# Kernel optimization log

Hardware: AMD Instinct MI355X
Metric: run time of the kernel (lower is better)

Reference implementation:

```python
import jax, jax.numpy as jnp
import numpy as np

IN_F = 4096
OUT_F = 4096
GROUPSIZE = 128
NUM_GROUPS = IN_F // GROUPSIZE  # 32


def setup_inputs() -> dict:
    key = jax.random.key(0)
    k1, k2, k3, k4 = jax.random.split(key, 4)
    x = jax.random.normal(k1, (4, 2048, IN_F), dtype=jnp.float32)
    imin = jnp.iinfo(jnp.int32).min
    imax = jnp.iinfo(jnp.int32).max
    qweight = jax.random.randint(k2, (IN_F // 8, OUT_F), imin, imax, dtype=jnp.int32)
    qzeros = jax.random.randint(k3, (NUM_GROUPS, OUT_F // 8), imin, imax, dtype=jnp.int32)
    scales = jax.random.uniform(k4, (NUM_GROUPS, OUT_F), dtype=jnp.float32,
                                minval=1e-3, maxval=2e-2)
    return {"x": x, "qweight": qweight, "qzeros": qzeros, "scales": scales}


def _unpack_rows(q):
    # q: int32 [in/8, out] -> float nibbles [in, out]; nibble i of a word is bits 4i..4i+3
    u = q.astype(jnp.uint32)
    shifts = (4 * jnp.arange(8, dtype=jnp.uint32))[None, :, None]  # [1,8,1]
    nib = (u[:, None, :] >> shifts) & jnp.uint32(0xF)              # [in/8, 8, out]
    return nib.reshape(q.shape[0] * 8, q.shape[1]).astype(jnp.float32)


def _unpack_cols(q):
    # q: int32 [g, out/8] -> float nibbles [g, out]
    u = q.astype(jnp.uint32)
    shifts = (4 * jnp.arange(8, dtype=jnp.uint32))[None, None, :]  # [1,1,8]
    nib = (u[:, :, None] >> shifts) & jnp.uint32(0xF)              # [g, out/8, 8]
    return nib.reshape(q.shape[0], q.shape[1] * 8).astype(jnp.float32)


def _dequant(qweight, qzeros, scales):
    # GPTQ dequant: w = scale[g] * (q - (z[g] + 1))
    q = _unpack_rows(qweight)                      # [IN_F, OUT_F]
    z = _unpack_cols(qzeros) + 1.0                 # [G, OUT_F]
    qg = q.reshape(NUM_GROUPS, GROUPSIZE, OUT_F)
    w = (qg - z[:, None, :]) * scales[:, None, :]
    return w.reshape(IN_F, OUT_F)


def reference(x, qweight, qzeros, scales):
    w = _dequant(qweight, qzeros, scales)          # [IN_F, OUT_F]
    # x: [B, S, IN_F] @ w -> [B, S, OUT_F]
    return jnp.einsum('bsi,io->bso', x, w)
```

## Files before the change

kernel.cpp:

```cpp
#include <hip/hip_runtime.h>
#include <stdint.h>

#define IN_F   4096
#define OUT_F  4096
#define M_ROWS 8192
#define KT     (IN_F / 64)

typedef __attribute__((ext_vector_type(8))) short  bf16x8;
typedef __attribute__((ext_vector_type(4))) float  f32x4;

__device__ __forceinline__ short f2bf(float f) {
    union { float f; uint32_t u; } v; v.f = f;
    uint32_t r = v.u + 0x7FFFu + ((v.u >> 16) & 1u);
    return (short)(r >> 16);
}

__device__ __forceinline__ void load_lds16(const void* gsrc, void* lds) {
    __builtin_amdgcn_global_load_lds(
        (const __attribute__((address_space(1))) uint32_t*)gsrc,
        (__attribute__((address_space(3))) uint32_t*)lds,
        16, 0, 0);
}

__global__ void dequant_wt_kernel(const int* __restrict__ qweight,
                                  const int* __restrict__ qzeros,
                                  const float* __restrict__ scales,
                                  short* __restrict__ wt)
{
    int t  = blockIdx.x * blockDim.x + threadIdx.x;
    int n  = t >> 9;
    int kw = t & 511;
    int g  = kw >> 4;

    float s = scales[g * OUT_F + n];
    uint32_t zw = (uint32_t)qzeros[g * (OUT_F / 8) + (n >> 3)];
    float z1 = (float)((zw >> (4 * (n & 7))) & 0xFu) + 1.0f;
    uint32_t q = (uint32_t)qweight[kw * OUT_F + n];

    bf16x8 out;
#pragma unroll
    for (int i = 0; i < 8; ++i) {
        float w = s * ((float)((q >> (4 * i)) & 0xFu) - z1);
        out[i] = f2bf(w);
    }
    *reinterpret_cast<bf16x8*>(&wt[(size_t)n * IN_F + kw * 8]) = out;
}

__global__ void xconv_kernel(const float* __restrict__ x, short* __restrict__ xb)
{
    int t = blockIdx.x * blockDim.x + threadIdx.x;
    const float4* src = reinterpret_cast<const float4*>(x) + (size_t)t * 2;
    float4 a = src[0], b = src[1];
    bf16x8 h;
    h[0] = f2bf(a.x); h[1] = f2bf(a.y); h[2] = f2bf(a.z); h[3] = f2bf(a.w);
    h[4] = f2bf(b.x); h[5] = f2bf(b.y); h[6] = f2bf(b.z); h[7] = f2bf(b.w);
    reinterpret_cast<bf16x8*>(xb)[t] = h;
}

__global__ __launch_bounds__(512, 2) void gemm8_kernel(
    const short* __restrict__ Xb,
    const short* __restrict__ WT,
    float* __restrict__ C)
{
    __shared__ short As[2][256 * 64];
    __shared__ short Bs[2][256 * 64];

    const int tid  = threadIdx.x;
    const int lane = tid & 63;
    const int wid  = tid >> 6;
    const int wr   = wid >> 2;
    const int wc   = wid & 3;

    const int row0 = blockIdx.y * 256;
    const int col0 = blockIdx.x * 256;

    const int rL0 = tid >> 3;
    const int csw = ((tid & 7) << 3) ^ ((rL0 & 7) << 3);
    const short* gA[4]; const short* gB[4]; int dOff[4];
#pragma unroll
    for (int L = 0; L < 4; ++L) {
        const int r = L * 64 + rL0;
        gA[L] = Xb + (size_t)(row0 + r) * IN_F + csw;
        gB[L] = WT + (size_t)(col0 + r) * IN_F + csw;
        dOff[L] = L * 8192 + tid * 16;
    }

    const int frow = lane & 15;
    const int k0   = ((lane >> 4) << 4) ^ ((frow & 7) << 4);

    f32x4 acc[8][4] = {};

#pragma unroll
    for (int L = 0; L < 4; ++L) load_lds16(gA[L], (char*)As[0] + dOff[L]);
#pragma unroll
    for (int L = 0; L < 4; ++L) load_lds16(gB[L], (char*)Bs[0] + dOff[L]);
    asm volatile("s_waitcnt vmcnt(0)" ::: "memory");
    __builtin_amdgcn_s_barrier();

    for (int t = 0; t < KT; ++t) {
        const int s = t & 1;
        char* Ab = (char*)As[s];
        char* Bb = (char*)Bs[s];
        char* An = (char*)As[s ^ 1];
        char* Bn = (char*)Bs[s ^ 1];
        const bool pf = (t < KT - 1);

#pragma unroll
        for (int q = 0; q < 4; ++q) {
            const int mq = q >> 1, nq = q & 1;

            bf16x8 af[4][2]; bf16x8 bfr[2][2];
#pragma unroll
            for (int m = 0; m < 4; ++m) {
                const int r = wr * 128 + (mq * 4 + m) * 16 + frow;
                char* base = Ab + r * 128;
                af[m][0] = *reinterpret_cast<const bf16x8*>(base + k0);
                af[m][1] = *reinterpret_cast<const bf16x8*>(base + (k0 ^ 64));
            }
#pragma unroll
            for (int n = 0; n < 2; ++n) {
                const int r = wc * 64 + (nq * 2 + n) * 16 + frow;
                char* base = Bb + r * 128;
                bfr[n][0] = *reinterpret_cast<const bf16x8*>(base + k0);
                bfr[n][1] = *reinterpret_cast<const bf16x8*>(base + (k0 ^ 64));
            }

            if (q == 0 && pf) {
#pragma unroll
                for (int L = 0; L < 4; ++L)
                    load_lds16(gA[L] + (size_t)(t + 1) * 64, An + dOff[L]);
            }
            if (q == 1 && pf) {
#pragma unroll
                for (int L = 0; L < 4; ++L)
                    load_lds16(gB[L] + (size_t)(t + 1) * 64, Bn + dOff[L]);
            }

            __builtin_amdgcn_s_barrier();
            asm volatile("s_waitcnt lgkmcnt(0)" ::: "memory");
            __builtin_amdgcn_sched_barrier(0);

            __builtin_amdgcn_s_setprio(1);
#pragma unroll
            for (int m = 0; m < 4; ++m)
#pragma unroll
                for (int n = 0; n < 2; ++n) {
                    acc[mq * 4 + m][nq * 2 + n] =
                        __builtin_amdgcn_mfma_f32_16x16x32_bf16(
                            af[m][0], bfr[n][0], acc[mq * 4 + m][nq * 2 + n], 0, 0, 0);
                    acc[mq * 4 + m][nq * 2 + n] =
                        __builtin_amdgcn_mfma_f32_16x16x32_bf16(
                            af[m][1], bfr[n][1], acc[mq * 4 + m][nq * 2 + n], 0, 0, 0);
                }
            __builtin_amdgcn_s_setprio(0);

            if (q == 3 && pf)
                asm volatile("s_waitcnt vmcnt(0)" ::: "memory");
            __builtin_amdgcn_s_barrier();
        }
    }

    const int crow = (lane >> 4) * 4;
    const int ccol = lane & 15;
#pragma unroll
    for (int fm = 0; fm < 8; ++fm)
#pragma unroll
        for (int fn = 0; fn < 4; ++fn)
#pragma unroll
            for (int r = 0; r < 4; ++r) {
                const int row = row0 + wr * 128 + fm * 16 + crow + r;
                const int col = col0 + wc * 64 + fn * 16 + ccol;
                C[(size_t)row * OUT_F + col] = acc[fm][fn][r];
            }
}

#define BM 128
#define BN 128
#define BK 64

__global__ __launch_bounds__(256, 2) void gemm_x_wt_kernel(
    const float* __restrict__ X,
    const short* __restrict__ WT,
    float* __restrict__ C)
{
    __shared__ short As2[BM * BK];
    __shared__ short Bs2[BN * BK];

    const int bn = blockIdx.x;
    const int bm = blockIdx.y;
    const int tid  = threadIdx.x;
    const int lane = tid & 63;
    const int wid  = tid >> 6;
    const int wr   = wid >> 1;
    const int wc   = wid & 1;

    const int row0 = bm * BM;
    const int col0 = bn * BN;
    const int frow = lane & 15;
    const int fk   = (lane >> 4) * 8;

    f32x4 acc[4][4] = {};

    for (int kt = 0; kt < IN_F / BK; ++kt) {
        float4 a0[4], a1[4];
#pragma unroll
        for (int j = 0; j < 4; ++j) {
            const int flat = (j * 256 + tid) * 8;
            const int r = flat >> 6;
            const int c = flat & (BK - 1);
            const float* src = X + (size_t)(row0 + r) * IN_F + kt * BK + c;
            a0[j] = *reinterpret_cast<const float4*>(src);
            a1[j] = *reinterpret_cast<const float4*>(src + 4);
        }
        __syncthreads();
#pragma unroll
        for (int j = 0; j < 4; ++j) {
            const int flat = (j * 256 + tid) * 8;
            const int r = flat >> 6;
            const int c = flat & (BK - 1);
            load_lds16(WT + (size_t)(col0 + r) * IN_F + kt * BK + c, &Bs2[flat]);
        }
#pragma unroll
        for (int j = 0; j < 4; ++j) {
            const int flat = (j * 256 + tid) * 8;
            bf16x8 h;
            h[0] = f2bf(a0[j].x); h[1] = f2bf(a0[j].y);
            h[2] = f2bf(a0[j].z); h[3] = f2bf(a0[j].w);
            h[4] = f2bf(a1[j].x); h[5] = f2bf(a1[j].y);
            h[6] = f2bf(a1[j].z); h[7] = f2bf(a1[j].w);
            *reinterpret_cast<bf16x8*>(&As2[flat]) = h;
        }
        __syncthreads();
#pragma unroll
        for (int s = 0; s < 2; ++s) {
            bf16x8 af[4], bfr[4];
#pragma unroll
            for (int m = 0; m < 4; ++m) {
                const int row = wr * 64 + m * 16 + frow;
                af[m] = *reinterpret_cast<const bf16x8*>(&As2[row * BK + s * 32 + fk]);
            }
#pragma unroll
            for (int n = 0; n < 4; ++n) {
                const int col = wc * 64 + n * 16 + frow;
                bfr[n] = *reinterpret_cast<const bf16x8*>(&Bs2[col * BK + s * 32 + fk]);
            }
#pragma unroll
            for (int m = 0; m < 4; ++m)
#pragma unroll
                for (int n = 0; n < 4; ++n)
                    acc[m][n] = __builtin_amdgcn_mfma_f32_16x16x32_bf16(
                        af[m], bfr[n], acc[m][n], 0, 0, 0);
        }
    }

    const int crow = (lane >> 4) * 4;
    const int ccol = lane & 15;
#pragma unroll
    for (int m = 0; m < 4; ++m)
#pragma unroll
        for (int n = 0; n < 4; ++n)
#pragma unroll
            for (int r = 0; r < 4; ++r) {
                const int row = row0 + wr * 64 + m * 16 + crow + r;
                const int col = col0 + wc * 64 + n * 16 + ccol;
                C[(size_t)row * OUT_F + col] = acc[m][n][r];
            }
}

extern "C" void kernel_launch(void* const* d_in, const int* in_sizes, int n_in,
                              void* d_out, int out_size, void* d_ws, size_t ws_size,
                              hipStream_t stream) {
    const float* x       = (const float*)d_in[0];
    const int*   qweight = (const int*)  d_in[1];
    const int*   qzeros  = (const int*)  d_in[2];
    const float* scales  = (const float*)d_in[3];
    float*       out     = (float*)d_out;

    const size_t WT_BYTES = (size_t)OUT_F * IN_F * 2;
    const size_t XB_BYTES = (size_t)M_ROWS * IN_F * 2;

    short* wt = (short*)d_ws;

    dequant_wt_kernel<<<(OUT_F * (IN_F / 8)) / 256, 256, 0, stream>>>(
        qweight, qzeros, scales, wt);

    if (ws_size >= WT_BYTES + XB_BYTES) {
        short* xb = (short*)((char*)d_ws + WT_BYTES);
        xconv_kernel<<<(M_ROWS * IN_F / 8) / 256, 256, 0, stream>>>(x, xb);
        dim3 grid(OUT_F / 256, M_ROWS / 256);
        gemm8_kernel<<<grid, 512, 0, stream>>>(xb, wt, out);
    } else {
        dim3 grid(OUT_F / BN, M_ROWS / BM);
        gemm_x_wt_kernel<<<grid, 256, 0, stream>>>(x, wt, out);
    }
}
```

Baseline: 318.1 us.

## Triple-buffer A tiles to prefetch two K-steps ahead in GEMM

Result: slower. 350.6 us (+10.2%).

```diff
diff --git a/kernel.cpp b/kernel.cpp
--- a/kernel.cpp
+++ b/kernel.cpp
@@ -57,13 +57,18 @@
     reinterpret_cast<bf16x8*>(xb)[t] = h;
 }
 
-__global__ __launch_bounds__(512, 2) void gemm8_kernel(
+#define A_SLOT 32768
+#define B_SLOT 32768
+
+__global__ __launch_bounds__(512, 1) void gemm8_kernel(
     const short* __restrict__ Xb,
     const short* __restrict__ WT,
     float* __restrict__ C)
 {
-    __shared__ short As[2][256 * 64];
-    __shared__ short Bs[2][256 * 64];
+    __shared__ short AsBuf[3 * 256 * 64];
+    __shared__ short BsBuf[2 * 256 * 64];
+    char* const Abase = (char*)AsBuf;
+    char* const Bbase = (char*)BsBuf;
 
     const int tid  = threadIdx.x;
     const int lane = tid & 63;
@@ -91,19 +96,25 @@
     f32x4 acc[8][4] = {};
 
 #pragma unroll
-    for (int L = 0; L < 4; ++L) load_lds16(gA[L], (char*)As[0] + dOff[L]);
-#pragma unroll
-    for (int L = 0; L < 4; ++L) load_lds16(gB[L], (char*)Bs[0] + dOff[L]);
-    asm volatile("s_waitcnt vmcnt(0)" ::: "memory");
+    for (int L = 0; L < 4; ++L) load_lds16(gA[L],      Abase + 0 * A_SLOT + dOff[L]);
+#pragma unroll
+    for (int L = 0; L < 4; ++L) load_lds16(gB[L],      Bbase + 0 * B_SLOT + dOff[L]);
+#pragma unroll
+    for (int L = 0; L < 4; ++L) load_lds16(gA[L] + 64, Abase + 1 * A_SLOT + dOff[L]);
+    asm volatile("s_waitcnt vmcnt(4)" ::: "memory");
     __builtin_amdgcn_s_barrier();
 
+    int sA = 0;
+    int sB = 0;
+
     for (int t = 0; t < KT; ++t) {
-        const int s = t & 1;
-        char* Ab = (char*)As[s];
-        char* Bb = (char*)Bs[s];
-        char* An = (char*)As[s ^ 1];
-        char* Bn = (char*)Bs[s ^ 1];
-        const bool pf = (t < KT - 1);
+        char* Ab = Abase + sA * A_SLOT;
+        char* Bb = Bbase + sB * B_SLOT;
+        const int sA2 = (sA >= 1) ? sA - 1 : 2;
+        char* An = Abase + sA2 * A_SLOT;
+        char* Bn = Bbase + (sB ^ 1) * B_SLOT;
+        const bool pfB = (t + 1 < KT);
+        const bool pfA = (t + 2 < KT);
 
 #pragma unroll
         for (int q = 0; q < 4; ++q) {
@@ -125,15 +136,15 @@
                 bfr[n][1] = *reinterpret_cast<const bf16x8*>(base + (k0 ^ 64));
             }
 
-            if (q == 0 && pf) {
-#pragma unroll
-                for (int L = 0; L < 4; ++L)
-                    load_lds16(gA[L] + (size_t)(t + 1) * 64, An + dOff[L]);
-            }
-            if (q == 1 && pf) {
+            if (q == 0 && pfB) {
 #pragma unroll
                 for (int L = 0; L < 4; ++L)
                     load_lds16(gB[L] + (size_t)(t + 1) * 64, Bn + dOff[L]);
+            }
+            if (q == 2 && pfA) {
+#pragma unroll
+                for (int L = 0; L < 4; ++L)
+                    load_lds16(gA[L] + (size_t)(t + 2) * 64, An + dOff[L]);
             }
 
             __builtin_amdgcn_s_barrier();
@@ -154,10 +165,15 @@
                 }
             __builtin_amdgcn_s_setprio(0);
 
-            if (q == 3 && pf)
-                asm volatile("s_waitcnt vmcnt(0)" ::: "memory");
+            if (q == 3) {
+                if (t < KT - 2)       asm volatile("s_waitcnt vmcnt(4)" ::: "memory");
+                else if (t == KT - 2) asm volatile("s_waitcnt vmcnt(0)" ::: "memory");
+            }
             __builtin_amdgcn_s_barrier();
         }
+
+        sA = (sA < 2) ? sA + 1 : 0;
+        sB ^= 1;
     }
 
     const int crow = (lane >> 4) * 4;
```
